# Kernel tuning notes

Measured on AMD Instinct MI355X. Metric: run time of the kernel, lower is better.

## Reference

```python
import jax, jax.numpy as jnp
import numpy as np

A, B, D = 64, 128, 256   # batch, route nodes, feature_dim
H, C = 64, 32            # hidden_capsule, center_num
NUM_ITERS = 3


def _squash(t, axis=-1):
    sq = jnp.sum(t * t, axis=axis, keepdims=True)
    return (sq / (1.0 + sq)) * t / jnp.sqrt(sq)


def _route(priors, n_iters):
    # priors: [K, A, R, D]; dynamic routing over axis=2 (R).
    # Original keeps logits of priors' full shape, but they stay constant
    # along D (init zeros, delta has keepdim on last axis), so [K,A,R,1]
    # is exactly equivalent and avoids a redundant [K,A,R,D] buffer.
    logits = jnp.zeros(priors.shape[:-1] + (1,), priors.dtype)
    outputs = None
    for i in range(n_iters):
        probs = jax.nn.softmax(logits, axis=2)          # [K,A,R,1]
        outputs = _squash(jnp.sum(probs * priors, axis=2, keepdims=True))  # [K,A,1,D]
        if i != n_iters - 1:
            logits = logits + jnp.sum(priors * outputs, axis=-1, keepdims=True)
    return outputs


def setup_inputs() -> dict:
    key = jax.random.key(0)
    k1, k2, k3 = jax.random.split(key, 3)
    x = jax.random.normal(k1, (A, B, D), dtype=jnp.float32)
    route_weights1 = jax.random.normal(k2, (H, D, D), dtype=jnp.float32)
    route_weights = jax.random.normal(k3, (C, D, D), dtype=jnp.float32)
    return {"x": x, "route_weights1": route_weights1, "route_weights": route_weights}


def reference(x, route_weights1, route_weights):
    # stage 1: priors1[h,a,b,:] = x[a,b,:] @ W1[h]  -> [H,A,B,D]
    priors1 = jnp.einsum('abd,hde->habe', x, route_weights1)
    out1 = _route(priors1, NUM_ITERS)                  # [H,A,1,D]
    out1 = jnp.transpose(out1[:, :, 0, :], (1, 0, 2))  # squeeze + transpose(0,1) -> [A,H,D]
    # stage 2: priors[c,a,h,:] = out1[a,h,:] @ W[c]   -> [C,A,H,D]
    priors = jnp.einsum('ahd,cde->cahe', out1, route_weights)
    out = _route(priors, NUM_ITERS)                    # [C,A,1,D]
    return out[:, :, 0, :]                             # squeeze -> [C,A,D]
```

## Files before the change

kernel.cpp:

```cpp
#include <hip/hip_runtime.h>
#include <hip/hip_bf16.h>

typedef __attribute__((ext_vector_type(8))) short bf16x8;
typedef __attribute__((ext_vector_type(4))) float f32x4;
typedef unsigned short u16;
typedef unsigned int u32;

__device__ __forceinline__ u32 bf16_rne(float f) {
  u32 u = __float_as_uint(f);
  return (u + 0x7FFFu + ((u >> 16) & 1u)) >> 16;
}
__device__ __forceinline__ float bf16_val(u32 b) { return __uint_as_float(b << 16); }

__device__ __forceinline__ void g2l16(const u16* g, u16* l) {
  __builtin_amdgcn_global_load_lds(
      (const __attribute__((address_space(1))) u32*)g,
      (__attribute__((address_space(3))) u32*)l, 16, 0, 0);
}

__global__ void split_arr(const float* __restrict__ in,
                          u16* __restrict__ hi, u16* __restrict__ lo, int n4) {
  int i = blockIdx.x * 256 + threadIdx.x;
  if (i >= n4) return;
  float4 v = ((const float4*)in)[i];
  u32 h0 = bf16_rne(v.x), h1 = bf16_rne(v.y), h2 = bf16_rne(v.z), h3 = bf16_rne(v.w);
  u32 l0 = bf16_rne(v.x - bf16_val(h0));
  u32 l1 = bf16_rne(v.y - bf16_val(h1));
  u32 l2 = bf16_rne(v.z - bf16_val(h2));
  u32 l3 = bf16_rne(v.w - bf16_val(h3));
  ushort4 hv; hv.x = (u16)h0; hv.y = (u16)h1; hv.z = (u16)h2; hv.w = (u16)h3;
  ushort4 lv; lv.x = (u16)l0; lv.y = (u16)l1; lv.z = (u16)l2; lv.w = (u16)l3;
  ((ushort4*)hi)[i] = hv;
  ((ushort4*)lo)[i] = lv;
}

__global__ void split_transpose256(const float* __restrict__ in,
                                   u16* __restrict__ hi, u16* __restrict__ lo) {
  __shared__ float tile[32][33];
  const size_t off = (size_t)blockIdx.z * 65536;
  const int tx = threadIdx.x, ty = threadIdx.y;
#pragma unroll
  for (int i = 0; i < 4; ++i) {
    int y = blockIdx.y * 32 + ty + i * 8;
    int x = blockIdx.x * 32 + tx;
    tile[ty + i * 8][tx] = in[off + (size_t)y * 256 + x];
  }
  __syncthreads();
#pragma unroll
  for (int i = 0; i < 4; ++i) {
    float v = tile[tx][ty + i * 8];
    u32 hb = bf16_rne(v);
    u32 lb = bf16_rne(v - bf16_val(hb));
    size_t idx = off + (size_t)(blockIdx.x * 32 + ty + i * 8) * 256 + blockIdx.y * 32 + tx;
    hi[idx] = (u16)hb;
    lo[idx] = (u16)lb;
  }
}

template <int R>
__global__ __launch_bounds__(256, 2) void caps_route(
    const u16* __restrict__ Ahi_g,
    const u16* __restrict__ Alo_g,
    const u16* __restrict__ Whi,
    const u16* __restrict__ Wlo,
    u16* __restrict__ o1hi, u16* __restrict__ o1lo,
    float* __restrict__ outp,
    int KN, int stage) {
  constexpr int APB = 128 / R;
  constexpr int SEG = APB;
  constexpr int MTS = 8 / SEG;
  constexpr int ABS = (R == 128) ? 6 : 5;
  __shared__ __align__(16) u16 Ab[2][8192];
  __shared__ __align__(16) u16 Wb[16384];
  __shared__ __align__(16) float wlog[4][128];
  __shared__ __align__(16) float probs[128];
  __shared__ float sqpart[2][4];

  const int tid = threadIdx.x;
  const int w = tid >> 6, lane = tid & 63, q = lane >> 4, li = lane & 15;
  const int eg = w;
  const int kk = blockIdx.x >> ABS;
  const int ab = blockIdx.x & ((1 << ABS) - 1);

  const int sub = lane >> 2, p = lane & 3;
  const int gslot = p ^ ((sub >> 1) & 3);
  const size_t lane_off = (size_t)sub * 256 + gslot * 8;
  const u16* gsrc;
  u16* ldst;
  if (w == 0)      { gsrc = Whi   + (size_t)kk * 65536 + lane_off; ldst = &Wb[0]       + lane * 8; }
  else if (w == 1) { gsrc = Wlo   + (size_t)kk * 65536 + lane_off; ldst = &Wb[8192]    + lane * 8; }
  else if (w == 2) { gsrc = Ahi_g + (size_t)ab * 32768 + lane_off; ldst = &Ab[0][0]    + lane * 8; }
  else             { gsrc = Alo_g + (size_t)ab * 32768 + lane_off; ldst = &Ab[0][4096] + lane * 8; }

  auto STAGE = [&](int ko, int nb) {
    if (w < 2) {
#pragma unroll
      for (int i = 0; i < 16; ++i) g2l16(gsrc + ko + i * 4096, ldst + i * 512);
    } else {
      u16* d = ldst + nb * 8192;
#pragma unroll
      for (int i = 0; i < 8; ++i) g2l16(gsrc + ko + i * 4096, d + i * 512);
    }
  };

  const int rslot = q ^ ((li >> 1) & 3);
  const int fbase = li * 32 + rslot * 8;

  f32x4 acc[8][4] = {};

  STAGE(0, 0);
  asm volatile("s_waitcnt vmcnt(0)" ::: "memory");
  __builtin_amdgcn_s_barrier();

#pragma unroll
  for (int ks = 0; ks < 8; ++ks) {
    bf16x8 bh[4], bl[4];
#pragma unroll
    for (int ct = 0; ct < 4; ++ct) {
      const u16* bp = &Wb[(eg * 4 + ct) * 512] + fbase;
      bh[ct] = *(const bf16x8*)bp;
      bl[ct] = *(const bf16x8*)(bp + 8192);
    }
    asm volatile("s_waitcnt lgkmcnt(0)" ::: "memory");
    __builtin_amdgcn_s_barrier();
    if (ks < 7) STAGE((ks + 1) * 32, (ks + 1) & 1);
    const u16* aB = &Ab[ks & 1][0] + fbase;
#pragma unroll
    for (int mt = 0; mt < 8; ++mt) {
      bf16x8 ah = *(const bf16x8*)(aB + mt * 512);
      bf16x8 al = *(const bf16x8*)(aB + mt * 512 + 4096);
#pragma unroll
      for (int ct = 0; ct < 4; ++ct) {
        acc[mt][ct] = __builtin_amdgcn_mfma_f32_16x16x32_bf16(al, bh[ct], acc[mt][ct], 0, 0, 0);
        acc[mt][ct] = __builtin_amdgcn_mfma_f32_16x16x32_bf16(ah, bl[ct], acc[mt][ct], 0, 0, 0);
        acc[mt][ct] = __builtin_amdgcn_mfma_f32_16x16x32_bf16(ah, bh[ct], acc[mt][ct], 0, 0, 0);
      }
    }
    asm volatile("s_waitcnt vmcnt(0)" ::: "memory");
    __builtin_amdgcn_s_barrier();
  }

  const float invR = 1.0f / R;
  float v[SEG][4];
  float lg0 = 0.f, lg1 = 0.f;

  for (int iter = 0; iter < 3; ++iter) {
    float4 p4[8];
    if (iter == 0) {
#pragma unroll
      for (int mt = 0; mt < 8; ++mt) {
        p4[mt].x = invR; p4[mt].y = invR; p4[mt].z = invR; p4[mt].w = invR;
      }
    } else {
#pragma unroll
      for (int mt = 0; mt < 8; ++mt)
        p4[mt] = *(const float4*)&probs[mt * 16 + q * 4];
    }
    float s[SEG][4];
#pragma unroll
    for (int sg = 0; sg < SEG; ++sg) {
#pragma unroll
      for (int ct = 0; ct < 4; ++ct) {
        float t = 0.f;
#pragma unroll
        for (int mi = 0; mi < MTS; ++mi) {
          const int mt = sg * MTS + mi;
          t += p4[mt].x * acc[mt][ct][0] + p4[mt].y * acc[mt][ct][1] +
               p4[mt].z * acc[mt][ct][2] + p4[mt].w * acc[mt][ct][3];
        }
        t += __shfl_xor(t, 16);
        t += __shfl_xor(t, 32);
        s[sg][ct] = t;
      }
    }
#pragma unroll
    for (int sg = 0; sg < SEG; ++sg) {
      float ss = s[sg][0] * s[sg][0] + s[sg][1] * s[sg][1] +
                 s[sg][2] * s[sg][2] + s[sg][3] * s[sg][3];
      ss += __shfl_xor(ss, 1); ss += __shfl_xor(ss, 2);
      ss += __shfl_xor(ss, 4); ss += __shfl_xor(ss, 8);
      if (lane == 0) sqpart[sg][eg] = ss;
    }
    __syncthreads();
#pragma unroll
    for (int sg = 0; sg < SEG; ++sg) {
      float sq = sqpart[sg][0] + sqpart[sg][1] + sqpart[sg][2] + sqpart[sg][3];
      float scale = (sq > 0.f) ? sq / ((1.0f + sq) * sqrtf(sq)) : 0.f;
#pragma unroll
      for (int ct = 0; ct < 4; ++ct) v[sg][ct] = s[sg][ct] * scale;
    }

    if (iter < 2) {
#pragma unroll
      for (int mt = 0; mt < 8; ++mt) {
        const int sg = mt / MTS;
        float tt[4];
#pragma unroll
        for (int rr = 0; rr < 4; ++rr) {
          float t = acc[mt][0][rr] * v[sg][0] + acc[mt][1][rr] * v[sg][1] +
                    acc[mt][2][rr] * v[sg][2] + acc[mt][3][rr] * v[sg][3];
          t += __shfl_xor(t, 1); t += __shfl_xor(t, 2);
          t += __shfl_xor(t, 4); t += __shfl_xor(t, 8);
          tt[rr] = t;
        }
        if (li == 0)
          *(float4*)&wlog[eg][mt * 16 + q * 4] = make_float4(tt[0], tt[1], tt[2], tt[3]);
      }
      __syncthreads();
      if (R == 128) {
        int r0 = lane, r1 = lane + 64;
        lg0 += wlog[0][r0] + wlog[1][r0] + wlog[2][r0] + wlog[3][r0];
        lg1 += wlog[0][r1] + wlog[1][r1] + wlog[2][r1] + wlog[3][r1];
        float m = fmaxf(lg0, lg1);
#pragma unroll
        for (int d2 = 1; d2 < 64; d2 <<= 1) m = fmaxf(m, __shfl_xor(m, d2));
        float e0 = __expf(lg0 - m), e1 = __expf(lg1 - m);
        float zz = e0 + e1;
#pragma unroll
        for (int d2 = 1; d2 < 64; d2 <<= 1) zz += __shfl_xor(zz, d2);
        float inv = 1.0f / zz;
        probs[r0] = e0 * inv;
        probs[r1] = e1 * inv;
      } else {
        int r0 = lane, r1 = lane + 64;
        lg0 += wlog[0][r0] + wlog[1][r0] + wlog[2][r0] + wlog[3][r0];
        lg1 += wlog[0][r1] + wlog[1][r1] + wlog[2][r1] + wlog[3][r1];
        float m0 = lg0, m1 = lg1;
#pragma unroll
        for (int d2 = 1; d2 < 64; d2 <<= 1) {
          m0 = fmaxf(m0, __shfl_xor(m0, d2));
          m1 = fmaxf(m1, __shfl_xor(m1, d2));
        }
        float e0 = __expf(lg0 - m0), e1 = __expf(lg1 - m1);
        float z0 = e0, z1 = e1;
#pragma unroll
        for (int d2 = 1; d2 < 64; d2 <<= 1) {
          z0 += __shfl_xor(z0, d2);
          z1 += __shfl_xor(z1, d2);
        }
        probs[r0] = e0 / z0;
        probs[r1] = e1 / z1;
      }
      asm volatile("s_waitcnt lgkmcnt(0)" ::: "memory");
    }
  }

  if (q == 0) {
#pragma unroll
    for (int sg = 0; sg < SEG; ++sg) {
      const int ag = ab * APB + sg;
      if (stage == 1) {
        size_t ob = ((size_t)ag * KN + kk) * 256;
#pragma unroll
        for (int ct = 0; ct < 4; ++ct) {
          int e = eg * 64 + ct * 16 + li;
          u32 hb = bf16_rne(v[sg][ct]);
          u32 lb = bf16_rne(v[sg][ct] - bf16_val(hb));
          o1hi[ob + e] = (u16)hb;
          o1lo[ob + e] = (u16)lb;
        }
      } else {
        size_t ob = ((size_t)kk * 64 + ag) * 256;
#pragma unroll
        for (int ct = 0; ct < 4; ++ct) {
          int e = eg * 64 + ct * 16 + li;
          outp[ob + e] = v[sg][ct];
        }
      }
    }
  }
}

extern "C" void kernel_launch(void* const* d_in, const int* in_sizes, int n_in,
                              void* d_out, int out_size, void* d_ws, size_t ws_size,
                              hipStream_t stream) {
  const float* x  = (const float*)d_in[0];
  const float* w1 = (const float*)d_in[1];
  const float* wc = (const float*)d_in[2];
  float* out = (float*)d_out;

  char* ws = (char*)d_ws;
  u16* w1hi = (u16*)(ws);
  u16* w1lo = (u16*)(ws + (8u << 20));
  u16* wchi = (u16*)(ws + (16u << 20));
  u16* wclo = (u16*)(ws + (20u << 20));
  u16* xhi  = (u16*)(ws + (24u << 20));
  u16* xlo  = (u16*)(ws + (28u << 20));
  u16* o1hi = (u16*)(ws + (32u << 20));
  u16* o1lo = (u16*)(ws + (34u << 20));

  split_arr<<<2048, 256, 0, stream>>>(x, xhi, xlo, 524288);
  split_transpose256<<<dim3(8, 8, 64), dim3(32, 8), 0, stream>>>(w1, w1hi, w1lo);
  split_transpose256<<<dim3(8, 8, 32), dim3(32, 8), 0, stream>>>(wc, wchi, wclo);
  caps_route<128><<<64 * 64, 256, 0, stream>>>(xhi, xlo, w1hi, w1lo, o1hi, o1lo, nullptr, 64, 1);
  caps_route<64><<<32 * 32, 256, 0, stream>>>(o1hi, o1lo, wchi, wclo, nullptr, nullptr, out, 32, 2);
}
```

Measured before the change: 357.2 us.

## Load W fragments directly into registers and drop the shared W buffer

The W hi/lo tiles are no longer staged through a 32KB shared buffer. Each lane now loads its B-fragments straight from global memory into registers, prefetching the next k-slice while the MFMAs run. The A staging is redistributed evenly across all four waves, and launch bounds are raised to 4 blocks per SIMD to use the freed LDS. The trade-off is uncoalesced 16-byte global loads of W and tighter register pressure under the higher occupancy bound, which may cause spills.

```diff
diff --git a/kernel.cpp b/kernel.cpp
--- a/kernel.cpp
+++ b/kernel.cpp
@@ -58,7 +58,7 @@
 }
 
 template <int R>
-__global__ __launch_bounds__(256, 2) void caps_route(
+__global__ __launch_bounds__(256, 4) void caps_route(
     const u16* __restrict__ Ahi_g,
     const u16* __restrict__ Alo_g,
     const u16* __restrict__ Whi,
@@ -71,7 +71,6 @@
   constexpr int MTS = 8 / SEG;
   constexpr int ABS = (R == 128) ? 6 : 5;
   __shared__ __align__(16) u16 Ab[2][8192];
-  __shared__ __align__(16) u16 Wb[16384];
   __shared__ __align__(16) float wlog[4][128];
   __shared__ __align__(16) float probs[128];
   __shared__ float sqpart[2][4];
@@ -85,45 +84,46 @@
   const int sub = lane >> 2, p = lane & 3;
   const int gslot = p ^ ((sub >> 1) & 3);
   const size_t lane_off = (size_t)sub * 256 + gslot * 8;
-  const u16* gsrc;
-  u16* ldst;
-  if (w == 0)      { gsrc = Whi   + (size_t)kk * 65536 + lane_off; ldst = &Wb[0]       + lane * 8; }
-  else if (w == 1) { gsrc = Wlo   + (size_t)kk * 65536 + lane_off; ldst = &Wb[8192]    + lane * 8; }
-  else if (w == 2) { gsrc = Ahi_g + (size_t)ab * 32768 + lane_off; ldst = &Ab[0][0]    + lane * 8; }
-  else             { gsrc = Alo_g + (size_t)ab * 32768 + lane_off; ldst = &Ab[0][4096] + lane * 8; }
+  const u16* gAh = Ahi_g + (size_t)ab * 32768 + (size_t)(2 * w) * 4096 + lane_off;
+  const u16* gAl = Alo_g + (size_t)ab * 32768 + (size_t)(2 * w) * 4096 + lane_off;
 
   auto STAGE = [&](int ko, int nb) {
-    if (w < 2) {
-#pragma unroll
-      for (int i = 0; i < 16; ++i) g2l16(gsrc + ko + i * 4096, ldst + i * 512);
-    } else {
-      u16* d = ldst + nb * 8192;
-#pragma unroll
-      for (int i = 0; i < 8; ++i) g2l16(gsrc + ko + i * 4096, d + i * 512);
-    }
+    u16* d = &Ab[nb][(2 * w) * 512] + lane * 8;
+    g2l16(gAh + ko, d);
+    g2l16(gAh + ko + 4096, d + 512);
+    g2l16(gAl + ko, d + 4096);
+    g2l16(gAl + ko + 4096, d + 4608);
   };
+
+  const u16* gWh = Whi + (size_t)kk * 65536 + (size_t)(eg * 64 + li) * 256 + q * 8;
+  const u16* gWl = Wlo + (size_t)kk * 65536 + (size_t)(eg * 64 + li) * 256 + q * 8;
 
   const int rslot = q ^ ((li >> 1) & 3);
   const int fbase = li * 32 + rslot * 8;
 
   f32x4 acc[8][4] = {};
 
+  bf16x8 bh[4], bl[4];
+#pragma unroll
+  for (int ct = 0; ct < 4; ++ct) {
+    bh[ct] = *(const bf16x8*)(gWh + ct * 4096);
+    bl[ct] = *(const bf16x8*)(gWl + ct * 4096);
+  }
   STAGE(0, 0);
   asm volatile("s_waitcnt vmcnt(0)" ::: "memory");
   __builtin_amdgcn_s_barrier();
 
 #pragma unroll
   for (int ks = 0; ks < 8; ++ks) {
-    bf16x8 bh[4], bl[4];
-#pragma unroll
-    for (int ct = 0; ct < 4; ++ct) {
-      const u16* bp = &Wb[(eg * 4 + ct) * 512] + fbase;
-      bh[ct] = *(const bf16x8*)bp;
-      bl[ct] = *(const bf16x8*)(bp + 8192);
-    }
-    asm volatile("s_waitcnt lgkmcnt(0)" ::: "memory");
-    __builtin_amdgcn_s_barrier();
-    if (ks < 7) STAGE((ks + 1) * 32, (ks + 1) & 1);
+    bf16x8 nbh[4], nbl[4];
+    if (ks < 7) {
+      STAGE((ks + 1) * 32, (ks + 1) & 1);
+#pragma unroll
+      for (int ct = 0; ct < 4; ++ct) {
+        nbh[ct] = *(const bf16x8*)(gWh + ct * 4096 + (ks + 1) * 32);
+        nbl[ct] = *(const bf16x8*)(gWl + ct * 4096 + (ks + 1) * 32);
+      }
+    }
     const u16* aB = &Ab[ks & 1][0] + fbase;
 #pragma unroll
     for (int mt = 0; mt < 8; ++mt) {
@@ -138,6 +138,10 @@
     }
     asm volatile("s_waitcnt vmcnt(0)" ::: "memory");
     __builtin_amdgcn_s_barrier();
+    if (ks < 7) {
+#pragma unroll
+      for (int ct = 0; ct < 4; ++ct) { bh[ct] = nbh[ct]; bl[ct] = nbl[ct]; }
+    }
   }
 
   const float invR = 1.0f / R;
```

After: 1.321 ms. +269.7%, slower.
